# Kernel tuning notes

Hardware: AMD Instinct MI355X
Metric: run time of the kernel (lower is better)

Reference implementation:

```python
import jax, jax.numpy as jnp
import numpy as np

N_NODES = 100000
N_EDGES = 1600000
F_IN = 100
HEADS = 3
HEAD_DIM = 64
HIDDEN = HEADS * HEAD_DIM  # 192
NUM_GRAPHS = 128
NUM_CLASSES = 2
NEG_SLOPE_ATT = 0.2   # PyG GATConv attention leaky_relu slope
NEG_SLOPE_ACT = 0.01  # F.leaky_relu default slope


def setup_inputs() -> dict:
    key = jax.random.key(0)
    ks = jax.random.split(key, 9)
    x = jax.random.normal(ks[0], (N_NODES, F_IN), dtype=jnp.float32)
    edge_index = jax.random.randint(ks[1], (2, N_EDGES), 0, N_NODES, dtype=jnp.int64)
    batch = jnp.sort(jax.random.randint(ks[2], (N_NODES,), 0, NUM_GRAPHS, dtype=jnp.int64))
    s = 0.05
    W = jax.random.normal(ks[3], (F_IN, HIDDEN), dtype=jnp.float32) * s
    att_src = jax.random.normal(ks[4], (HEADS, HEAD_DIM), dtype=jnp.float32) * s
    att_dst = jax.random.normal(ks[5], (HEADS, HEAD_DIM), dtype=jnp.float32) * s
    bias = jax.random.normal(ks[6], (HIDDEN,), dtype=jnp.float32) * s
    cls_W = jax.random.normal(ks[7], (HIDDEN, NUM_CLASSES), dtype=jnp.float32) * s
    cls_b = jax.random.normal(ks[8], (NUM_CLASSES,), dtype=jnp.float32) * s
    return {"x": x, "edge_index": edge_index, "batch": batch, "W": W,
            "att_src": att_src, "att_dst": att_dst, "bias": bias,
            "cls_W": cls_W, "cls_b": cls_b}


def _gat_forward(x, edge_index, batch, W, att_src, att_dst, bias, cls_W, cls_b):
    N = x.shape[0]
    # PyG GATConv adds self-loops by default
    loops = jnp.arange(N, dtype=edge_index.dtype)
    src = jnp.concatenate([edge_index[0], loops])
    dst = jnp.concatenate([edge_index[1], loops])

    h = (x @ W).reshape(N, HEADS, HEAD_DIM)          # [N,H,C]
    a_src = jnp.sum(h * att_src, axis=-1)            # [N,H]
    a_dst = jnp.sum(h * att_dst, axis=-1)            # [N,H]

    e = a_src[src] + a_dst[dst]                      # [Etot,H]
    e = jax.nn.leaky_relu(e, NEG_SLOPE_ATT)

    # segment softmax over incoming edges of each destination node
    m = jax.ops.segment_max(e, dst, num_segments=N)  # [N,H]
    e = jnp.exp(e - m[dst])
    denom = jax.ops.segment_sum(e, dst, num_segments=N)
    alpha = e / denom[dst]                           # [Etot,H]

    msg = h[src] * alpha[:, :, None]                 # [Etot,H,C]
    out = jax.ops.segment_sum(msg, dst, num_segments=N).reshape(N, HIDDEN) + bias

    out = jax.nn.leaky_relu(out, NEG_SLOPE_ACT)      # F.leaky_relu (dropout inactive: eval)
    pooled = jax.ops.segment_max(out, batch, num_segments=NUM_GRAPHS)  # global_max_pool
    return pooled @ cls_W + cls_b                    # [NUM_GRAPHS, NUM_CLASSES]


def reference(x, edge_index, batch, W, att_src, att_dst, bias, cls_W, cls_b):
    return _gat_forward(x, edge_index, batch, W, att_src, att_dst, bias, cls_W, cls_b)
```

## Files before the change

### kernel.cpp

```cpp
#include <hip/hip_runtime.h>
#include <math.h>

#define N_NODES   100000
#define N_EDGES   1600000
#define ETOT      1700000
#define F_IN      100
#define HEADS     3
#define HEAD_DIM  64
#define HIDDEN    192
#define NUM_GRAPHS 128
#define NUM_CLASSES 2
#define WT_COLS   208
#define KPAD      128
#define NCHUNK    ((ETOT + 1023) / 1024)
#define DRANGE    (N_NODES / 8)
#define NGEMM     (N_NODES / 32)
#define OSTRIDE   200
#define GAGG      16
#define CAP       64

typedef unsigned short ushort_t;
typedef __attribute__((ext_vector_type(8))) short short8;
typedef __attribute__((ext_vector_type(4))) float floatx4;

__device__ __forceinline__ unsigned f2ord(float f) {
    unsigned u = __float_as_uint(f);
    return (u & 0x80000000u) ? ~u : (u | 0x80000000u);
}
__device__ __forceinline__ float ord2f(unsigned u) {
    return __uint_as_float((u & 0x80000000u) ? (u & 0x7fffffffu) : ~u);
}
__device__ __forceinline__ unsigned bf16rn(float f) {
    unsigned u = __float_as_uint(f);
    return (u + 0x7fffu + ((u >> 16) & 1u)) >> 16;
}

__global__ __launch_bounds__(256) void k_prep(
        const float* __restrict__ W, const float* __restrict__ att_src,
        const float* __restrict__ att_dst,
        ushort_t* __restrict__ WT_hi, ushort_t* __restrict__ WT_lo) {
    const int c0 = blockIdx.x * 8;
    const int t = threadIdx.x;
    __shared__ float wsv_s[F_IN * 6];
    if (c0 < HIDDEN + 6 && c0 + 8 > HIDDEN) {
        for (int p = t; p < F_IN * 6; p += 256) {
            int k = p / 6, j = p % 6;
            const float* a = (j < 3) ? att_src : att_dst;
            int hh = j % 3;
            float s = 0.f;
            for (int c = 0; c < HEAD_DIM; c++)
                s += W[k * HIDDEN + hh * HEAD_DIM + c] * a[hh * HEAD_DIM + c];
            wsv_s[p] = s;
        }
        __syncthreads();
    }
    for (int idx = t; idx < 8 * KPAD; idx += 256) {
        int col = c0 + (idx >> 7), k = idx & (KPAD - 1);
        float v = 0.f;
        if (k < F_IN) {
            if (col < HIDDEN) v = W[k * HIDDEN + col];
            else if (col < HIDDEN + 6) v = wsv_s[k * 6 + (col - HIDDEN)];
        }
        unsigned hi = bf16rn(v);
        WT_hi[col * KPAD + k] = (ushort_t)hi;
        float lo = v - __uint_as_float(hi << 16);
        WT_lo[col * KPAD + k] = (ushort_t)bf16rn(lo);
    }
}

__global__ __launch_bounds__(256) void k_mega(
        const float* __restrict__ x,
        const ushort_t* __restrict__ WT_hi, const ushort_t* __restrict__ WT_lo,
        ushort_t* __restrict__ hb,
        float* __restrict__ asrc, float* __restrict__ adst,
        const int* __restrict__ ei, int* __restrict__ count,
        int* __restrict__ srcs) {
    __shared__ ushort_t lds[32 * 136 * 2];
    const int tid = threadIdx.x;

    if (blockIdx.x >= NGEMM) {
        const int cls = blockIdx.x & 7;
        const int chunk = (blockIdx.x - NGEMM) >> 3;
        const int dlo = cls * DRANGE, dhi = dlo + DRANGE;
        const int base = chunk * 1024 + tid;
        int d4[4], s4[4];
#pragma unroll
        for (int q = 0; q < 4; q++) {
            int j = base + q * 256;
            if (j >= ETOT) { d4[q] = -1; s4[q] = 0; continue; }
            d4[q] = (j < N_EDGES) ? ei[N_EDGES + j] : (j - N_EDGES);
            s4[q] = (j < N_EDGES) ? ei[j] : d4[q];
        }
#pragma unroll
        for (int q = 0; q < 4; q++) {
            int d = d4[q];
            if (d < dlo || d >= dhi) continue;
            int pos = atomicAdd(&count[d], 1);
            if (pos < CAP) srcs[d * CAP + pos] = s4[q];
        }
        return;
    }

    ushort_t* xs_hi = lds;
    ushort_t* xs_lo = lds + 32 * 136;
    const int base = blockIdx.x * 32;
    for (int idx = tid; idx < 32 * KPAD; idx += 256) {
        int row = idx >> 7, k = idx & (KPAD - 1);
        float v = (k < F_IN) ? x[(base + row) * F_IN + k] : 0.f;
        unsigned hi = bf16rn(v);
        xs_hi[row * 136 + k] = (ushort_t)hi;
        float lo = v - __uint_as_float(hi << 16);
        xs_lo[row * 136 + k] = (ushort_t)bf16rn(lo);
    }
    __syncthreads();

    const int wid = tid >> 6, l = tid & 63;
    const int row16 = l & 15, g = l >> 4;
    const int NT = (wid == 3) ? 4 : 3;
    const int t0 = wid * 3;

    floatx4 acc[2][4];
#pragma unroll
    for (int m = 0; m < 2; m++)
#pragma unroll
        for (int i = 0; i < 4; i++) acc[m][i] = (floatx4)0.f;

#pragma unroll
    for (int c = 0; c < 4; c++) {
        const int ke = g * 8 + c * 32;
        short8 ah0 = *(const short8*)(xs_hi + row16 * 136 + ke);
        short8 al0 = *(const short8*)(xs_lo + row16 * 136 + ke);
        short8 ah1 = *(const short8*)(xs_hi + (16 + row16) * 136 + ke);
        short8 al1 = *(const short8*)(xs_lo + (16 + row16) * 136 + ke);
#pragma unroll
        for (int ti = 0; ti < 4; ti++) {
            if (ti >= NT) break;
            const int col = (t0 + ti) * 16 + row16;
            short8 bh = *(const short8*)(WT_hi + col * KPAD + ke);
            short8 bl = *(const short8*)(WT_lo + col * KPAD + ke);
            acc[0][ti] = __builtin_amdgcn_mfma_f32_16x16x32_bf16(ah0, bh, acc[0][ti], 0, 0, 0);
            acc[0][ti] = __builtin_amdgcn_mfma_f32_16x16x32_bf16(ah0, bl, acc[0][ti], 0, 0, 0);
            acc[0][ti] = __builtin_amdgcn_mfma_f32_16x16x32_bf16(al0, bh, acc[0][ti], 0, 0, 0);
            acc[1][ti] = __builtin_amdgcn_mfma_f32_16x16x32_bf16(ah1, bh, acc[1][ti], 0, 0, 0);
            acc[1][ti] = __builtin_amdgcn_mfma_f32_16x16x32_bf16(ah1, bl, acc[1][ti], 0, 0, 0);
            acc[1][ti] = __builtin_amdgcn_mfma_f32_16x16x32_bf16(al1, bh, acc[1][ti], 0, 0, 0);
        }
    }

    __syncthreads();

#pragma unroll
    for (int ti = 0; ti < 4; ti++) {
        if (ti >= NT) break;
        const int tile = t0 + ti;
        if (tile < 12) {
#pragma unroll
            for (int m = 0; m < 2; m++)
#pragma unroll
                for (int r = 0; r < 4; r++) {
                    int node = m * 16 + g * 4 + r;
                    lds[node * OSTRIDE + tile * 16 + row16] =
                        (ushort_t)bf16rn(acc[m][ti][r]);
                }
        } else if (row16 < 6) {
#pragma unroll
            for (int m = 0; m < 2; m++)
#pragma unroll
                for (int r = 0; r < 4; r++) {
                    int node = base + m * 16 + g * 4 + r;
                    if (row16 < 3) asrc[node * HEADS + row16] = acc[m][ti][r];
                    else           adst[node * HEADS + (row16 - 3)] = acc[m][ti][r];
                }
        }
    }
    __syncthreads();

    uint4* hb4 = (uint4*)(hb + (size_t)base * HIDDEN);
#pragma unroll
    for (int i = 0; i < 3; i++) {
        int q = tid + i * 256;
        int row = q / 24, c8 = q % 24;
        hb4[q] = *(const uint4*)(lds + row * OSTRIDE + c8 * 8);
    }
}

__global__ __launch_bounds__(192) void k_aggr(const int* __restrict__ count,
        const int* __restrict__ srcs, const float* __restrict__ asrc,
        const float* __restrict__ adst, const ushort_t* __restrict__ hb,
        const float* __restrict__ bias, const int* __restrict__ batch,
        unsigned* __restrict__ pooled) {
    __shared__ float sm[HIDDEN];
    const int n0 = blockIdx.x * GAGG;
    const int tid = threadIdx.x;
    const int head = tid >> 6, lane = tid & 63;
    const char* hbase = (const char*)hb + head * 128 + (lane & 7) * 16;
    const int src0 = lane >> 3;
    const int c0 = head * HEAD_DIM + (lane & 7) * 8;

    int cntv = (lane < GAGG) ? count[n0 + lane] : 0;
    int bgv  = (lane < GAGG) ? batch[n0 + lane] : 0;
    float adv = (lane < GAGG * HEADS) ? adst[n0 * HEADS + lane] : 0.f;
    float bv[8];
#pragma unroll
    for (int k = 0; k < 8; k++) bv[k] = bias[c0 + k];

    float vmax[8];
#pragma unroll
    for (int k = 0; k < 8; k++) vmax[k] = -INFINITY;
    int curg = __shfl(bgv, 0);

    for (int g = 0; g < GAGG; g++) {
        const int gg = __shfl(bgv, g);
        if (gg != curg) {
            if (lane < 8) {
#pragma unroll
                for (int k = 0; k < 8; k++) sm[c0 + k] = vmax[k];
            }
            __syncthreads();
            atomicMax(&pooled[curg * HIDDEN + tid], f2ord(sm[tid]));
            __syncthreads();
#pragma unroll
            for (int k = 0; k < 8; k++) vmax[k] = -INFINITY;
            curg = gg;
        }

        int cnt = __shfl(cntv, g);
        if (cnt > CAP) cnt = CAP;
        const float ad = __shfl(adv, g * HEADS + head);
        const int n = n0 + g;

        int s = srcs[n * CAP + lane];
        float myexp = 0.f; int myoff = 0;
        if (lane < cnt) {
            float e = asrc[s * HEADS + head] + ad;
            e = (e > 0.f) ? e : 0.2f * e;
            myexp = expf(e);
            myoff = s * (HIDDEN * 2);
        }

        float dsum = myexp;
#pragma unroll
        for (int m = 1; m < 64; m <<= 1) dsum += __shfl_xor(dsum, m);

        float acc[8];
#pragma unroll
        for (int k = 0; k < 8; k++) acc[k] = 0.f;
        int groups = (cnt + 7) >> 3;
#pragma unroll 2
        for (int j = 0; j < groups; j++) {
            int sl = j * 8 + src0;
            float a   = __shfl(myexp, sl);
            int   off = __shfl(myoff, sl);
            uint4 u = *(const uint4*)(hbase + off);
            acc[0] += a * __uint_as_float(u.x << 16);
            acc[1] += a * __uint_as_float(u.x & 0xffff0000u);
            acc[2] += a * __uint_as_float(u.y << 16);
            acc[3] += a * __uint_as_float(u.y & 0xffff0000u);
            acc[4] += a * __uint_as_float(u.z << 16);
            acc[5] += a * __uint_as_float(u.z & 0xffff0000u);
            acc[6] += a * __uint_as_float(u.w << 16);
            acc[7] += a * __uint_as_float(u.w & 0xffff0000u);
        }

#pragma unroll
        for (int k = 0; k < 8; k++) {
            acc[k] += __shfl_xor(acc[k], 8);
            acc[k] += __shfl_xor(acc[k], 16);
            acc[k] += __shfl_xor(acc[k], 32);
        }

        if (lane < 8) {
            const float inv = 1.f / dsum;
#pragma unroll
            for (int k = 0; k < 8; k++) {
                float v = acc[k] * inv + bv[k];
                v = (v > 0.f) ? v : 0.01f * v;
                vmax[k] = fmaxf(vmax[k], v);
            }
        }
    }

    if (lane < 8) {
#pragma unroll
        for (int k = 0; k < 8; k++) sm[c0 + k] = vmax[k];
    }
    __syncthreads();
    atomicMax(&pooled[curg * HIDDEN + tid], f2ord(sm[tid]));
}

__global__ __launch_bounds__(64) void k_cls(const unsigned* __restrict__ pooled,
        const float* __restrict__ clsW, const float* __restrict__ clsb,
        float* __restrict__ out) {
    const int g = blockIdx.x, lane = threadIdx.x;
    float s0 = 0.f, s1 = 0.f;
#pragma unroll
    for (int i = 0; i < 3; i++) {
        int f = i * 64 + lane;
        float pv = ord2f(pooled[g * HIDDEN + f]);
        s0 += pv * clsW[f * NUM_CLASSES];
        s1 += pv * clsW[f * NUM_CLASSES + 1];
    }
#pragma unroll
    for (int m = 1; m < 64; m <<= 1) {
        s0 += __shfl_xor(s0, m);
        s1 += __shfl_xor(s1, m);
    }
    if (lane == 0) {
        out[g * NUM_CLASSES]     = s0 + clsb[0];
        out[g * NUM_CLASSES + 1] = s1 + clsb[1];
    }
}

extern "C" void kernel_launch(void* const* d_in, const int* in_sizes, int n_in,
                              void* d_out, int out_size, void* d_ws, size_t ws_size,
                              hipStream_t stream) {
    const float* x       = (const float*)d_in[0];
    const int*   ei      = (const int*)d_in[1];
    const int*   batch   = (const int*)d_in[2];
    const float* W       = (const float*)d_in[3];
    const float* att_src = (const float*)d_in[4];
    const float* att_dst = (const float*)d_in[5];
    const float* bias    = (const float*)d_in[6];
    const float* clsW    = (const float*)d_in[7];
    const float* clsb    = (const float*)d_in[8];
    float* out = (float*)d_out;

    char* p = (char*)d_ws;
    auto alloc = [&](size_t bytes) {
        char* r = p; p += (bytes + 255) & ~size_t(255); return r;
    };
    ushort_t* hb     = (ushort_t*)alloc(sizeof(ushort_t) * N_NODES * HIDDEN);
    float*    asrc   = (float*)   alloc(sizeof(float) * N_NODES * HEADS);
    float*    adst   = (float*)   alloc(sizeof(float) * N_NODES * HEADS);
    int*      count  = (int*)     alloc(sizeof(int) * N_NODES);
    int*      srcs   = (int*)     alloc(sizeof(int) * (size_t)N_NODES * CAP);
    ushort_t* WT_hi  = (ushort_t*)alloc(sizeof(ushort_t) * WT_COLS * KPAD);
    ushort_t* WT_lo  = (ushort_t*)alloc(sizeof(ushort_t) * WT_COLS * KPAD);
    unsigned* pooled = (unsigned*)alloc(sizeof(unsigned) * NUM_GRAPHS * HIDDEN);

    hipMemsetAsync(count, 0, sizeof(int) * N_NODES, stream);
    hipMemsetAsync(pooled, 0, sizeof(unsigned) * NUM_GRAPHS * HIDDEN, stream);

    k_prep<<<WT_COLS / 8, 256, 0, stream>>>(W, att_src, att_dst, WT_hi, WT_lo);
    k_mega<<<NGEMM + NCHUNK * 8, 256, 0, stream>>>(x, WT_hi, WT_lo, hb, asrc, adst,
                                                   ei, count, srcs);
    k_aggr<<<N_NODES / GAGG, 192, 0, stream>>>(count, srcs, asrc, adst, hb, bias,
                                               batch, pooled);
    k_cls<<<NUM_GRAPHS, 64, 0, stream>>>(pooled, clsW, clsb, out);
}
```

Before: 373.1 us.

## Map aggregation threads to feature columns with scalar readlane edge loop

```diff
diff --git a/kernel.cpp b/kernel.cpp
--- a/kernel.cpp
+++ b/kernel.cpp
@@ -34,6 +34,12 @@
     unsigned u = __float_as_uint(f);
     return (u + 0x7fffu + ((u >> 16) & 1u)) >> 16;
 }
+__device__ __forceinline__ int rl_i(int v, int l) {
+    return __builtin_amdgcn_readlane(v, l);
+}
+__device__ __forceinline__ float rl_f(float v, int l) {
+    return __uint_as_float((unsigned)__builtin_amdgcn_readlane((int)__float_as_uint(v), l));
+}
 
 __global__ __launch_bounds__(256) void k_prep(
         const float* __restrict__ W, const float* __restrict__ att_src,
@@ -189,103 +195,55 @@
         const float* __restrict__ adst, const ushort_t* __restrict__ hb,
         const float* __restrict__ bias, const int* __restrict__ batch,
         unsigned* __restrict__ pooled) {
-    __shared__ float sm[HIDDEN];
     const int n0 = blockIdx.x * GAGG;
     const int tid = threadIdx.x;
     const int head = tid >> 6, lane = tid & 63;
-    const char* hbase = (const char*)hb + head * 128 + (lane & 7) * 16;
-    const int src0 = lane >> 3;
-    const int c0 = head * HEAD_DIM + (lane & 7) * 8;
 
     int cntv = (lane < GAGG) ? count[n0 + lane] : 0;
     int bgv  = (lane < GAGG) ? batch[n0 + lane] : 0;
     float adv = (lane < GAGG * HEADS) ? adst[n0 * HEADS + lane] : 0.f;
-    float bv[8];
-#pragma unroll
-    for (int k = 0; k < 8; k++) bv[k] = bias[c0 + k];
-
-    float vmax[8];
-#pragma unroll
-    for (int k = 0; k < 8; k++) vmax[k] = -INFINITY;
-    int curg = __shfl(bgv, 0);
+    const float bv = bias[tid];
+
+    float vmax = -INFINITY;
+    int curg = rl_i(bgv, 0);
 
     for (int g = 0; g < GAGG; g++) {
-        const int gg = __shfl(bgv, g);
+        const int gg = rl_i(bgv, g);
         if (gg != curg) {
-            if (lane < 8) {
-#pragma unroll
-                for (int k = 0; k < 8; k++) sm[c0 + k] = vmax[k];
-            }
-            __syncthreads();
-            atomicMax(&pooled[curg * HIDDEN + tid], f2ord(sm[tid]));
-            __syncthreads();
-#pragma unroll
-            for (int k = 0; k < 8; k++) vmax[k] = -INFINITY;
+            atomicMax(&pooled[curg * HIDDEN + tid], f2ord(vmax));
+            vmax = -INFINITY;
             curg = gg;
         }
 
-        int cnt = __shfl(cntv, g);
+        int cnt = rl_i(cntv, g);
         if (cnt > CAP) cnt = CAP;
-        const float ad = __shfl(adv, g * HEADS + head);
+        const float ad = rl_f(adv, g * HEADS + head);
         const int n = n0 + g;
 
-        int s = srcs[n * CAP + lane];
-        float myexp = 0.f; int myoff = 0;
+        int sv = 0; float myexp = 0.f;
         if (lane < cnt) {
-            float e = asrc[s * HEADS + head] + ad;
+            sv = srcs[n * CAP + lane];
+            float e = asrc[sv * HEADS + head] + ad;
             e = (e > 0.f) ? e : 0.2f * e;
             myexp = expf(e);
-            myoff = s * (HIDDEN * 2);
-        }
-
-        float dsum = myexp;
-#pragma unroll
-        for (int m = 1; m < 64; m <<= 1) dsum += __shfl_xor(dsum, m);
-
-        float acc[8];
-#pragma unroll
-        for (int k = 0; k < 8; k++) acc[k] = 0.f;
-        int groups = (cnt + 7) >> 3;
-#pragma unroll 2
-        for (int j = 0; j < groups; j++) {
-            int sl = j * 8 + src0;
-            float a   = __shfl(myexp, sl);
-            int   off = __shfl(myoff, sl);
-            uint4 u = *(const uint4*)(hbase + off);
-            acc[0] += a * __uint_as_float(u.x << 16);
-            acc[1] += a * __uint_as_float(u.x & 0xffff0000u);
-            acc[2] += a * __uint_as_float(u.y << 16);
-            acc[3] += a * __uint_as_float(u.y & 0xffff0000u);
-            acc[4] += a * __uint_as_float(u.z << 16);
-            acc[5] += a * __uint_as_float(u.z & 0xffff0000u);
-            acc[6] += a * __uint_as_float(u.w << 16);
-            acc[7] += a * __uint_as_float(u.w & 0xffff0000u);
-        }
-
-#pragma unroll
-        for (int k = 0; k < 8; k++) {
-            acc[k] += __shfl_xor(acc[k], 8);
-            acc[k] += __shfl_xor(acc[k], 16);
-            acc[k] += __shfl_xor(acc[k], 32);
-        }
-
-        if (lane < 8) {
-            const float inv = 1.f / dsum;
-#pragma unroll
-            for (int k = 0; k < 8; k++) {
-                float v = acc[k] * inv + bv[k];
-                v = (v > 0.f) ? v : 0.01f * v;
-                vmax[k] = fmaxf(vmax[k], v);
-            }
-        }
-    }
-
-    if (lane < 8) {
-#pragma unroll
-        for (int k = 0; k < 8; k++) sm[c0 + k] = vmax[k];
-    }
-    __syncthreads();
-    atomicMax(&pooled[curg * HIDDEN + tid], f2ord(sm[tid]));
+        }
+
+        float acc = 0.f, dsum = 0.f;
+#pragma unroll 4
+        for (int j = 0; j < cnt; j++) {
+            float a  = rl_f(myexp, j);
+            int   sj = rl_i(sv, j);
+            float hv = __uint_as_float((unsigned)hb[(size_t)sj * HIDDEN + tid] << 16);
+            acc  += a * hv;
+            dsum += a;
+        }
+
+        float v = acc * (1.f / dsum) + bv;
+        v = (v > 0.f) ? v : 0.01f * v;
+        vmax = fmaxf(vmax, v);
+    }
+
+    atomicMax(&pooled[curg * HIDDEN + tid], f2ord(vmax));
 }
 
 __global__ __launch_bounds__(64) void k_cls(const unsigned* __restrict__ pooled,
```

Result: slower. 543.6 us (+45.7%).
